# Optimization experiments

Measured on AMD Instinct MI355X. Metric: run time of the kernel, lower is better.

Reference implementation:

```python
import jax, jax.numpy as jnp
import numpy as np

D_MODEL = 768
N_HEADS = 12
D_HEAD = 64
WINDOW = 16
LOOK_BACK = 1
IGNORE = -1.0e6


def look_around(x, backward=LOOK_BACK, forward=0, pad_value=0):
    # x: (b, n_windows, w, ...) -> (b, n_windows, w*(backward+forward+1), ...)
    n = x.shape[1]
    pad = [(0, 0)] * x.ndim
    pad[1] = (backward, forward)
    px = jnp.pad(x, pad, constant_values=pad_value)
    return jnp.concatenate([px[:, i:i + n] for i in range(backward + forward + 1)], axis=2)


def setup_inputs() -> dict:
    key = jax.random.key(0)
    k1, k2, k3 = jax.random.split(key, 3)
    B, T = 2, 2048
    x = jax.random.normal(k1, (B, T, D_MODEL), dtype=jnp.float32)
    W_abcde = jax.random.normal(k2, (D_MODEL, 5 * N_HEADS * D_HEAD), dtype=jnp.float32) * (1.0 / np.sqrt(D_MODEL))
    b_abcde = jnp.zeros((5 * N_HEADS * D_HEAD,), dtype=jnp.float32)
    W_O = jax.random.normal(k3, (N_HEADS * D_HEAD, D_MODEL), dtype=jnp.float32) * (1.0 / np.sqrt(N_HEADS * D_HEAD))
    b_O = jnp.zeros((D_MODEL,), dtype=jnp.float32)
    return {"x": x, "W_abcde": W_abcde, "b_abcde": b_abcde, "W_O": W_O, "b_O": b_O}


def reference(x, W_abcde, b_abcde, W_O, b_O):
    B, T, _ = x.shape
    w = WINDOW
    nw = T // w
    Ww = w * (LOOK_BACK + 1)  # look-around window length

    abcde = x @ W_abcde + b_abcde                                    # (B,T,5*H*D)
    abcde = abcde.reshape(B, T, 5, N_HEADS, D_HEAD).transpose(2, 0, 3, 1, 4)  # (5,B,H,T,D)
    a, b, c, d, e = [t.reshape(B * N_HEADS, nw, w, D_HEAD) for t in abcde]
    a_l, b_l, d_l, e_l = (look_around(t) for t in (a, b, d, e))       # (BH,nw,Ww,D)

    # causal mask, same construction as get_causal_mask (pad_value=0)
    seq = jnp.arange(T).reshape(1, nw, w)
    bb = look_around(seq)                                            # (1,nw,Ww)
    # mask[n,m,l] = (seq_n < bb_l) | (bb_l <= bb_m)
    mask = (seq[..., :, None, None] < bb[..., None, None, :]) | (bb[..., None, None, :] <= bb[..., None, :, None])

    # third-order attention scores: (BH, nw, w, Ww, Ww)
    scores = jnp.einsum('bnwd,bnmd,bnld->bnwml', c, a_l, b_l)
    scores = jnp.where(mask, IGNORE, scores)
    scores = jnp.where(scores == 0, IGNORE, scores)
    probs = jax.nn.softmax((scores / D_HEAD).reshape(B * N_HEADS, nw, w, Ww * Ww), axis=-1)
    probs = probs.reshape(scores.shape)

    z = jnp.einsum('bnwml,bnmd->bnwd', probs, d_l) + jnp.einsum('bnwml,bnld->bnwd', probs, e_l)
    z = z.reshape(B, N_HEADS, nw, w, D_HEAD).transpose(0, 2, 3, 1, 4).reshape(B, T, N_HEADS * D_HEAD)
    return z @ W_O + b_O
```

## Files before the change

### kernel.cpp

```cpp
#include <hip/hip_runtime.h>

#define T_SEQ   2048
#define NHEADS  12
#define DHEAD   64
#define WIN     16
#define WW      32
#define NWIN    128
#define DMODEL  768
#define NABCDE  3840
#define IGNORE_V (-1.0e6f)
#define PAD_K   72
#define L2E64   0.022542110013890053f
#define IGN_SC  (-22542.110013890053f)

typedef float f32x4 __attribute__((ext_vector_type(4)));
typedef _Float16 f16x8 __attribute__((ext_vector_type(8)));

__device__ __forceinline__ short f2h(float f) {
    union { _Float16 h; short s; } u;
    u.h = (_Float16)f;
    return u.s;
}

__device__ __forceinline__ void gload_lds16(const short* g, short* l) {
    __builtin_amdgcn_global_load_lds(
        (const __attribute__((address_space(1))) void*)g,
        (__attribute__((address_space(3))) void*)l,
        16, 0, 0);
}

__global__ __launch_bounds__(256) void prep_kernel(
    const float* __restrict__ x, const float* __restrict__ W_abcde,
    const float* __restrict__ W_O,
    short* __restrict__ xh, short* __restrict__ Wt, short* __restrict__ WOt)
{
    __shared__ float tile[32][33];
    const int blk = blockIdx.x;
    const int tid = threadIdx.x;

    if (blk < 1536) {
        int i = (blk * 256 + tid) * 8;
        float4 a = *reinterpret_cast<const float4*>(&x[i]);
        float4 b = *reinterpret_cast<const float4*>(&x[i + 4]);
        union { short s[8]; uint4 u; } r;
        r.s[0] = f2h(a.x); r.s[1] = f2h(a.y); r.s[2] = f2h(a.z); r.s[3] = f2h(a.w);
        r.s[4] = f2h(b.x); r.s[5] = f2h(b.y); r.s[6] = f2h(b.z); r.s[7] = f2h(b.w);
        *reinterpret_cast<uint4*>(&xh[i]) = r.u;
        return;
    }
    const float* W; short* Wo; int N, bx, by;
    if (blk < 4416) {
        int t = blk - 1536;
        W = W_abcde; Wo = Wt; N = NABCDE;
        bx = (t % 120) * 32; by = (t / 120) * 32;
    } else {
        int t = blk - 4416;
        W = W_O; Wo = WOt; N = DMODEL;
        bx = (t % 24) * 32; by = (t / 24) * 32;
    }
    const int tx = tid & 31, ty = tid >> 5;
#pragma unroll
    for (int r = 0; r < 32; r += 8)
        tile[ty + r][tx] = W[(size_t)(by + ty + r) * N + bx + tx];
    __syncthreads();
#pragma unroll
    for (int r = 0; r < 32; r += 8)
        Wo[(size_t)(bx + ty + r) * DMODEL + by + tx] = f2h(tile[tx][ty + r]);
}

__global__ __launch_bounds__(512, 2) void gemm1_kernel(
    const short* __restrict__ A, const short* __restrict__ Bt,
    const float* __restrict__ bias, short* __restrict__ C,
    int M, int N, int K)
{
    __shared__ short LT[4][2][8192];

    const int tid  = threadIdx.x;
    const int wave = tid >> 6;
    const int lane = tid & 63;

    int bid = blockIdx.x;
    int t = (bid & 7) * 30 + (bid >> 3);
    const int bm = (t / 15) * 256;
    const int bn = (t % 15) * 256;

    const int wr = wave >> 2;
    const int wc = wave & 3;
    const int fm = lane & 15;
    const int ko = lane >> 4;
    const int kswz = ko ^ ((lane >> 2) & 3);
    const int w32 = wave * 32;

    const int srow = lane >> 2;
    const int scc  = ((lane & 3) ^ ((lane >> 4) & 3)) * 8;
    const short* gA[2]; const short* gB[2];
#pragma unroll
    for (int j = 0; j < 2; ++j) {
        gA[j] = A  + (size_t)(bm + w32 + j * 16 + srow) * K + scc;
        gB[j] = Bt + (size_t)(bn + w32 + j * 16 + srow) * K + scc;
    }

    f32x4 acc[8][4];
#pragma unroll
    for (int mi = 0; mi < 8; ++mi)
#pragma unroll
        for (int ni = 0; ni < 4; ++ni) acc[mi][ni] = (f32x4){0.f, 0.f, 0.f, 0.f};

#pragma unroll
    for (int kt = 0; kt < 3; ++kt) {
#pragma unroll
        for (int j = 0; j < 2; ++j) {
            gload_lds16(gA[j] + kt * 32, &LT[kt][0][(w32 + j * 16) * 32]);
            gload_lds16(gB[j] + kt * 32, &LT[kt][1][(w32 + j * 16) * 32]);
        }
    }

    const int NKT = K >> 5;
    const int nkm = NKT - 3;

#define G1_STEP(KB, VMC, DOSTAGE, KS)                                          \
    {                                                                          \
        asm volatile("s_waitcnt vmcnt(" #VMC ")" ::: "memory");                \
        __builtin_amdgcn_s_barrier();                                          \
        asm volatile("" ::: "memory");                                         \
        if (DOSTAGE) {                                                         \
            int sb_ = (KS) & 3;                                                \
            _Pragma("unroll")                                                  \
            for (int j = 0; j < 2; ++j) {                                      \
                gload_lds16(gA[j] + (KS) * 32, &LT[sb_][0][(w32 + j * 16) * 32]); \
                gload_lds16(gB[j] + (KS) * 32, &LT[sb_][1][(w32 + j * 16) * 32]); \
            }                                                                  \
        }                                                                      \
        const short* Ab_ = &LT[(KB)][0][0];                                    \
        const short* Bb_ = &LT[(KB)][1][0];                                    \
        f16x8 af_[8], bf_[4];                                                  \
        _Pragma("unroll")                                                      \
        for (int mi = 0; mi < 8; ++mi)                                         \
            af_[mi] = *reinterpret_cast<const f16x8*>(                         \
                &Ab_[(wr * 128 + mi * 16 + fm) * 32 + kswz * 8]);              \
        _Pragma("unroll")                                                      \
        for (int ni = 0; ni < 4; ++ni)                                         \
            bf_[ni] = *reinterpret_cast<const f16x8*>(                         \
                &Bb_[(wc * 64 + ni * 16 + fm) * 32 + kswz * 8]);               \
        __builtin_amdgcn_s_setprio(1);                                         \
        _Pragma("unroll")                                                      \
        for (int mi = 0; mi < 8; ++mi)                                         \
            _Pragma("unroll")                                                  \
            for (int ni = 0; ni < 4; ++ni)                                     \
                acc[mi][ni] = __builtin_amdgcn_mfma_f32_16x16x32_f16(          \
                    af_[mi], bf_[ni], acc[mi][ni], 0, 0, 0);                   \
        __builtin_amdgcn_s_setprio(0);                                         \
        asm volatile("" ::: "memory");                                         \
        __builtin_amdgcn_s_barrier();                                          \
    }

    for (int k = 0; k < nkm; ++k) {
        G1_STEP(k & 3, 8, true, k + 3);
    }
    G1_STEP(nkm & 3, 8, false, 0);
    G1_STEP((nkm + 1) & 3, 4, false, 0);
    G1_STEP((nkm + 2) & 3, 0, false, 0);
#undef G1_STEP

    float bv[4];
#pragma unroll
    for (int ni = 0; ni < 4; ++ni)
        bv[ni] = bias[bn + wc * 64 + ni * 16 + fm];

    short* cb = &LT[0][0][0];
#pragma unroll
    for (int half = 0; half < 2; ++half) {
        __syncthreads();
        if (wr == half) {
#pragma unroll
            for (int mi = 0; mi < 8; ++mi) {
#pragma unroll
                for (int r = 0; r < 4; ++r) {
                    int lrow = mi * 16 + ko * 4 + r;
#pragma unroll
                    for (int ni = 0; ni < 4; ++ni)
                        cb[lrow * 256 + wc * 64 + ni * 16 + fm] =
                            f2h(acc[mi][ni][r] + bv[ni]);
                }
            }
        }
        __syncthreads();
#pragma unroll
        for (int q = 0; q < 8; ++q) {
            int f = tid + q * 512;
            int row = f >> 5, c16 = (f & 31) * 8;
            *reinterpret_cast<uint4*>(
                &C[(size_t)(bm + half * 128 + row) * N + bn + c16]) =
                *reinterpret_cast<const uint4*>(&cb[row * 256 + c16]);
        }
    }
}

__global__ __launch_bounds__(256) void gemm_h16_64(
    const short* __restrict__ A, const short* __restrict__ Bt,
    const float* __restrict__ bias, float* __restrict__ C,
    int M, int N, int K)
{
    __shared__ short As[2][64 * 32];
    __shared__ short Bs[2][64 * 32];

    const int tid  = threadIdx.x;
    const int wave = tid >> 6;
    const int lane = tid & 63;
    const int bm = blockIdx.y * 64;
    const int bn = blockIdx.x * 64;

    const int st_row = lane >> 2;
    const int st_col = (lane & 3) * 8;
    const int fr_m = lane & 15;
    const int fr_k = (lane >> 4) * 8;
    const int wm = wave * 16;

    const short* gsrc[4];
    short* ldst[4];
#pragma unroll
    for (int j = 0; j < 4; ++j) {
        int c = wave * 4 + j;
        if (c < 8) {
            int kt = c >> 2, rg = c & 3;
            gsrc[j] = A + (size_t)(bm + rg * 16 + st_row) * K + kt * 32 + st_col;
            ldst[j] = &As[kt][(rg * 16) * 32];
        } else {
            int cb = c - 8;
            int kt = cb >> 2, rg = cb & 3;
            gsrc[j] = Bt + (size_t)(bn + rg * 16 + st_row) * K + kt * 32 + st_col;
            ldst[j] = &Bs[kt][(rg * 16) * 32];
        }
    }

    f32x4 acc[4];
#pragma unroll
    for (int ni = 0; ni < 4; ++ni) acc[ni] = (f32x4){0.f, 0.f, 0.f, 0.f};

    for (int k0 = 0; k0 < K; k0 += 64) {
#pragma unroll
        for (int j = 0; j < 4; ++j) gload_lds16(gsrc[j] + k0, ldst[j]);
        __syncthreads();

#pragma unroll
        for (int kt = 0; kt < 2; ++kt) {
            f16x8 af = *reinterpret_cast<const f16x8*>(
                &As[kt][(wm + fr_m) * 32 + fr_k]);
#pragma unroll
            for (int ni = 0; ni < 4; ++ni) {
                f16x8 bf = *reinterpret_cast<const f16x8*>(
                    &Bs[kt][(ni * 16 + fr_m) * 32 + fr_k]);
                acc[ni] = __builtin_amdgcn_mfma_f32_16x16x32_f16(
                    af, bf, acc[ni], 0, 0, 0);
            }
        }
        __syncthreads();
    }

    float bv[4];
#pragma unroll
    for (int ni = 0; ni < 4; ++ni)
        bv[ni] = bias[bn + ni * 16 + (lane & 15)];
    int rbase = bm + wm + (lane >> 4) * 4;
#pragma unroll
    for (int r = 0; r < 4; ++r) {
        size_t off = (size_t)(rbase + r) * N + bn + (lane & 15);
#pragma unroll
        for (int ni = 0; ni < 4; ++ni)
            C[off + ni * 16] = acc[ni][r] + bv[ni];
    }
}

__global__ __launch_bounds__(256) void attn_kernel(
    const short* __restrict__ abcde, short* __restrict__ z)
{
    const int blk = blockIdx.x;
    const int n  = blk & (NWIN - 1);
    const int bh = blk >> 7;
    const int b  = bh / NHEADS;
    const int h  = bh % NHEADS;

    __shared__ short sc[WIN * PAD_K];
    __shared__ short sa[WW * PAD_K];
    __shared__ short sb[WW * PAD_K];
    __shared__ short sd[WW * PAD_K];
    __shared__ short se[WW * PAD_K];
    __shared__ short epA[WIN * PAD_K];
    __shared__ float sinv[WIN];

    const int tid = threadIdx.x;
    const size_t rowbase = ((size_t)b * T_SEQ) * NABCDE;
    const int hd = h * DHEAD;

    if (tid < 128) {
        int row = tid >> 3, ch = (tid & 7) * 8;
        *reinterpret_cast<uint4*>(&sc[row * PAD_K + ch]) =
            *reinterpret_cast<const uint4*>(
                &abcde[rowbase + (size_t)(n * WIN + row) * NABCDE + 2 * DMODEL + hd + ch]);
    }
    {
        int row = tid >> 3, ch = (tid & 7) * 8;
        int t = n * WIN - WIN + row;
        uint4 va = {0u, 0u, 0u, 0u}, vb = va, vd = va, ve = va;
        if (t >= 0) {
            size_t base = rowbase + (size_t)t * NABCDE + hd + ch;
            va = *reinterpret_cast<const uint4*>(&abcde[base + 0 * DMODEL]);
            vb = *reinterpret_cast<const uint4*>(&abcde[base + 1 * DMODEL]);
            vd = *reinterpret_cast<const uint4*>(&abcde[base + 3 * DMODEL]);
            ve = *reinterpret_cast<const uint4*>(&abcde[base + 4 * DMODEL]);
        }
        *reinterpret_cast<uint4*>(&sa[row * PAD_K + ch]) = va;
        *reinterpret_cast<uint4*>(&sb[row * PAD_K + ch]) = vb;
        *reinterpret_cast<uint4*>(&sd[row * PAD_K + ch]) = vd;
        *reinterpret_cast<uint4*>(&se[row * PAD_K + ch]) = ve;
    }
    __syncthreads();

    const int wv = tid >> 6;
    const int lane = tid & 63;
    const int lc = lane & 15;
    const int ko = lane >> 4;

    f16x8 cfrag[2];
    f16x8 bfrag[2][2];
#pragma unroll
    for (int kt = 0; kt < 2; ++kt) {
        cfrag[kt] = *reinterpret_cast<const f16x8*>(
            &sc[(wv * 4 + (lc & 3)) * PAD_K + kt * 32 + ko * 8]) * (_Float16)L2E64;
        bfrag[0][kt] = *reinterpret_cast<const f16x8*>(&sb[lc * PAD_K + kt * 32 + ko * 8]);
        bfrag[1][kt] = *reinterpret_cast<const f16x8*>(&sb[(16 + lc) * PAD_K + kt * 32 + ko * 8]);
    }

    f32x4 acc[8][2];
#pragma unroll
    for (int mt = 0; mt < 8; ++mt) {
        acc[mt][0] = (f32x4){0.f, 0.f, 0.f, 0.f};
        acc[mt][1] = (f32x4){0.f, 0.f, 0.f, 0.f};
    }
    __builtin_amdgcn_s_setprio(1);
#pragma unroll
    for (int mt = 0; mt < 8; ++mt) {
#pragma unroll
        for (int kt = 0; kt < 2; ++kt) {
            f16x8 ar = *reinterpret_cast<const f16x8*>(
                &sa[(mt * 4 + (lc >> 2)) * PAD_K + kt * 32 + ko * 8]);
            f16x8 pa = cfrag[kt] * ar;
            acc[mt][0] = __builtin_amdgcn_mfma_f32_16x16x32_f16(pa, bfrag[0][kt], acc[mt][0], 0, 0, 0);
            acc[mt][1] = __builtin_amdgcn_mfma_f32_16x16x32_f16(pa, bfrag[1][kt], acc[mt][1], 0, 0, 0);
        }
    }
    __builtin_amdgcn_s_setprio(0);

    const int nbase = n * WIN;
    if (n != 0) {
#pragma unroll
        for (int lt = 0; lt < 2; ++lt) {
            const int l = lt * 16 + lc;
#pragma unroll
            for (int mt = 0; mt < 8; ++mt) {
                const bool mgt = l > (mt * 4 + ko);
#pragma unroll
                for (int reg = 0; reg < 4; ++reg) {
                    const bool keep = mgt && (wv * 4 + reg + WIN >= l);
                    float p = __builtin_amdgcn_exp2f(acc[mt][lt][reg]);
                    acc[mt][lt][reg] = keep ? p : 0.0f;
                }
            }
        }
    } else {
        int bbl_h[2]; bool keepL[2][4];
#pragma unroll
        for (int lt = 0; lt < 2; ++lt) {
            int l = lt * 16 + lc;
            bbl_h[lt] = (l < WIN) ? 0 : (l - WIN);
#pragma unroll
            for (int reg = 0; reg < 4; ++reg)
                keepL[lt][reg] = (wv * 4 + reg) >= bbl_h[lt];
        }
#pragma unroll
        for (int mt = 0; mt < 8; ++mt) {
            int m = mt * 4 + ko;
            int bbm = (m < WIN) ? 0 : (m - WIN);
#pragma unroll
            for (int lt = 0; lt < 2; ++lt) {
                bool mgt = bbl_h[lt] > bbm;
#pragma unroll
                for (int reg = 0; reg < 4; ++reg) {
                    float s = acc[mt][lt][reg];
                    if (!(keepL[lt][reg] && mgt) || s == 0.0f)
                        acc[mt][lt][reg] = IGN_SC;
                }
            }
        }
        float mx[4] = {-3.4e38f, -3.4e38f, -3.4e38f, -3.4e38f};
#pragma unroll
        for (int mt = 0; mt < 8; ++mt)
#pragma unroll
            for (int lt = 0; lt < 2; ++lt)
#pragma unroll
                for (int reg = 0; reg < 4; ++reg)
                    mx[reg] = fmaxf(mx[reg], acc[mt][lt][reg]);
#pragma unroll
        for (int reg = 0; reg < 4; ++reg) {
#pragma unroll
            for (int off = 1; off < 64; off <<= 1)
                mx[reg] = fmaxf(mx[reg], __shfl_xor(mx[reg], off, 64));
        }
#pragma unroll
        for (int mt = 0; mt < 8; ++mt)
#pragma unroll
            for (int lt = 0; lt < 2; ++lt)
#pragma unroll
                for (int reg = 0; reg < 4; ++reg)
                    acc[mt][lt][reg] = __builtin_amdgcn_exp2f(
                        acc[mt][lt][reg] - mx[reg]);
    }

    float plv[2][4];
#pragma unroll
    for (int lt = 0; lt < 2; ++lt) {
#pragma unroll
        for (int reg = 0; reg < 4; ++reg) {
            float p = acc[0][lt][reg];
#pragma unroll
            for (int mt = 1; mt < 8; ++mt) p += acc[mt][lt][reg];
            p += __shfl_xor(p, 16, 64);
            p += __shfl_xor(p, 32, 64);
            plv[lt][reg] = p;
        }
        float w  = (ko & 1) ? plv[lt][1] : plv[lt][0];
        float w2 = (ko & 1) ? plv[lt][3] : plv[lt][2];
        float ww = (ko & 2) ? w2 : w;
        epA[(wv * 4 + ko) * PAD_K + 32 + lt * 16 + lc] = f2h(ww);
    }

    {
        float s[4];
#pragma unroll
        for (int reg = 0; reg < 4; ++reg) {
            float t = plv[0][reg] + plv[1][reg];
            t += __shfl_xor(t, 1, 64);
            t += __shfl_xor(t, 2, 64);
            t += __shfl_xor(t, 4, 64);
            t += __shfl_xor(t, 8, 64);
            s[reg] = t;
        }
        if (lane == 0) {
#pragma unroll
            for (int reg = 0; reg < 4; ++reg) sinv[wv * 4 + reg] = 1.0f / s[reg];
        }
    }

    {
        float v8[8][4];
#pragma unroll
        for (int mt = 0; mt < 8; ++mt)
#pragma unroll
            for (int reg = 0; reg < 4; ++reg)
                v8[mt][reg] = acc[mt][0][reg] + acc[mt][1][reg];

        const bool s0 = lane & 1, s1 = lane & 2, s2 = lane & 4, s3 = lane & 8;
        float r1[4][4];
#pragma unroll
        for (int m2 = 0; m2 < 4; ++m2)
#pragma unroll
            for (int reg = 0; reg < 4; ++reg) {
                float u = v8[2 * m2][reg], w = v8[2 * m2 + 1][reg];
                float a = s0 ? w : u;
                float s = s0 ? u : w;
                r1[m2][reg] = a + __shfl_xor(s, 1, 64);
            }
        float r2[2][4];
#pragma unroll
        for (int m4 = 0; m4 < 2; ++m4)
#pragma unroll
            for (int reg = 0; reg < 4; ++reg) {
                float u = r1[2 * m4][reg], w = r1[2 * m4 + 1][reg];
                float a = s1 ? w : u;
                float s = s1 ? u : w;
                r2[m4][reg] = a + __shfl_xor(s, 2, 64);
            }
        float r3[4];
#pragma unroll
        for (int reg = 0; reg < 4; ++reg) {
            float u = r2[0][reg], w = r2[1][reg];
            float a = s2 ? w : u;
            float s = s2 ? u : w;
            r3[reg] = a + __shfl_xor(s, 4, 64);
        }
        float a0 = s3 ? r3[1] : r3[0];
        float q0 = s3 ? r3[0] : r3[1];
        float g0 = a0 + __shfl_xor(q0, 8, 64);
        float a1 = s3 ? r3[3] : r3[2];
        float q1 = s3 ? r3[2] : r3[3];
        float g1 = a1 + __shfl_xor(q1, 8, 64);

        int mcol = (lc & 7) * 4 + ko;
        int ib = wv * 4 + (lc >> 3);
        epA[ib * PAD_K + mcol]       = f2h(g0);
        epA[(ib + 2) * PAD_K + mcol] = f2h(g1);
    }

    const int dd = wv * 16 + lc;
    f16x8 bd, be;
    {
        unsigned dv[8], ev[8];
#pragma unroll
        for (int j = 0; j < 8; ++j) {
            dv[j] = *reinterpret_cast<const unsigned short*>(&sd[(ko * 8 + j) * PAD_K + dd]);
            ev[j] = *reinterpret_cast<const unsigned short*>(&se[(ko * 8 + j) * PAD_K + dd]);
        }
        union { unsigned u[4]; f16x8 v; } td, te;
#pragma unroll
        for (int j = 0; j < 4; ++j) {
            td.u[j] = __builtin_amdgcn_perm(dv[2 * j + 1], dv[2 * j], 0x05040100);
            te.u[j] = __builtin_amdgcn_perm(ev[2 * j + 1], ev[2 * j], 0x05040100);
        }
        bd = td.v; be = te.v;
    }
    __syncthreads();

    f16x8 apm = *reinterpret_cast<const f16x8*>(&epA[lc * PAD_K + ko * 8]);
    f16x8 apl = *reinterpret_cast<const f16x8*>(&epA[lc * PAD_K + 32 + ko * 8]);
    f32x4 zacc = (f32x4){0.f, 0.f, 0.f, 0.f};
    __builtin_amdgcn_s_setprio(1);
    zacc = __builtin_amdgcn_mfma_f32_16x16x32_f16(apm, bd, zacc, 0, 0, 0);
    zacc = __builtin_amdgcn_mfma_f32_16x16x32_f16(apl, be, zacc, 0, 0, 0);
    __builtin_amdgcn_s_setprio(0);

    short* zs = sd;
#pragma unroll
    for (int reg = 0; reg < 4; ++reg) {
        int i = ko * 4 + reg;
        zs[i * 64 + dd] = f2h(zacc[reg] * sinv[i]);
    }
    __syncthreads();
    {
        int row = tid >> 4;
        int ch  = (tid & 15) * 4;
        *reinterpret_cast<uint2*>(
            &z[((size_t)b * T_SEQ + nbase + row) * (NHEADS * DHEAD) + hd + ch]) =
            *reinterpret_cast<const uint2*>(&zs[row * 64 + ch]);
    }
}

extern "C" void kernel_launch(void* const* d_in, const int* in_sizes, int n_in,
                              void* d_out, int out_size, void* d_ws, size_t ws_size,
                              hipStream_t stream) {
    const float* x        = (const float*)d_in[0];
    const float* W_abcde  = (const float*)d_in[1];
    const float* b_abcde  = (const float*)d_in[2];
    const float* W_O      = (const float*)d_in[3];
    const float* b_O      = (const float*)d_in[4];
    float* out = (float*)d_out;

    char* ws = (char*)d_ws;
    short* abcde = (short*)ws;
    short* xh    = (short*)(ws + (size_t)31457280);
    short* Wt    = (short*)(ws + (size_t)31457280 + 6291456);
    short* WOt   = (short*)(ws + (size_t)31457280 + 6291456 + 5898240);
    short* zb    = xh;

    const int M = 2 * T_SEQ;

    prep_kernel<<<dim3(4992), dim3(256), 0, stream>>>(
        x, W_abcde, W_O, xh, Wt, WOt);

    gemm1_kernel<<<dim3(240), dim3(512), 0, stream>>>(
        xh, Wt, b_abcde, abcde, M, NABCDE, DMODEL);

    attn_kernel<<<dim3(2 * NHEADS * NWIN), dim3(256), 0, stream>>>(abcde, zb);

    gemm_h16_64<<<dim3(DMODEL / 64, M / 64), dim3(256), 0, stream>>>(
        zb, WOt, b_O, out, M, DMODEL, DMODEL);
}
```

Before: 147.9 us.

## Rewrite output projection GEMM with 128x64 tiles and 4-stage LDS pipeline

Replaces the 64x64 output-projection GEMM with a 128x64 tile kernel that keeps three k-slices in flight in a four-buffer LDS ring, using explicit vmcnt waits and barriers. It adds an XOR swizzle on LDS columns to avoid bank conflicts, a block-index remap for cache locality, and raises MFMA priority. The aim is to hide global-load latency and raise MFMA work per LDS read. In exchange it launches fewer blocks (384 vs 768), which can reduce occupancy, and it relies on hand-counted waitcnt values.

```diff
diff --git a/kernel.cpp b/kernel.cpp
--- a/kernel.cpp
+++ b/kernel.cpp
@@ -196,78 +196,116 @@
     }
 }
 
-__global__ __launch_bounds__(256) void gemm_h16_64(
+__global__ __launch_bounds__(256) void gemm2_kernel(
     const short* __restrict__ A, const short* __restrict__ Bt,
     const float* __restrict__ bias, float* __restrict__ C,
     int M, int N, int K)
 {
-    __shared__ short As[2][64 * 32];
-    __shared__ short Bs[2][64 * 32];
+    __shared__ short LT[4][6144];
 
     const int tid  = threadIdx.x;
     const int wave = tid >> 6;
     const int lane = tid & 63;
-    const int bm = blockIdx.y * 64;
-    const int bn = blockIdx.x * 64;
-
-    const int st_row = lane >> 2;
-    const int st_col = (lane & 3) * 8;
-    const int fr_m = lane & 15;
-    const int fr_k = (lane >> 4) * 8;
-    const int wm = wave * 16;
-
-    const short* gsrc[4];
-    short* ldst[4];
-#pragma unroll
-    for (int j = 0; j < 4; ++j) {
-        int c = wave * 4 + j;
+
+    int bid = blockIdx.x;
+    int t = (bid & 7) * 48 + (bid >> 3);
+    const int bm = (t / 12) * 128;
+    const int bn = (t % 12) * 64;
+
+    const int wr = wave >> 1;
+    const int wc = wave & 1;
+    const int fm = lane & 15;
+    const int ko = lane >> 4;
+    const int kswz = ko ^ ((lane >> 2) & 3);
+
+    const int srow = lane >> 2;
+    const int scc  = ((lane & 3) ^ ((lane >> 4) & 3)) * 8;
+
+    const short* gsrc[3];
+    int loff[3];
+#pragma unroll
+    for (int j = 0; j < 3; ++j) {
+        int c = wave * 3 + j;
         if (c < 8) {
-            int kt = c >> 2, rg = c & 3;
-            gsrc[j] = A + (size_t)(bm + rg * 16 + st_row) * K + kt * 32 + st_col;
-            ldst[j] = &As[kt][(rg * 16) * 32];
+            gsrc[j] = A + (size_t)(bm + c * 16 + srow) * K + scc;
+            loff[j] = (c * 16) * 32;
         } else {
             int cb = c - 8;
-            int kt = cb >> 2, rg = cb & 3;
-            gsrc[j] = Bt + (size_t)(bn + rg * 16 + st_row) * K + kt * 32 + st_col;
-            ldst[j] = &Bs[kt][(rg * 16) * 32];
-        }
-    }
-
-    f32x4 acc[4];
-#pragma unroll
-    for (int ni = 0; ni < 4; ++ni) acc[ni] = (f32x4){0.f, 0.f, 0.f, 0.f};
-
-    for (int k0 = 0; k0 < K; k0 += 64) {
-#pragma unroll
-        for (int j = 0; j < 4; ++j) gload_lds16(gsrc[j] + k0, ldst[j]);
-        __syncthreads();
-
-#pragma unroll
-        for (int kt = 0; kt < 2; ++kt) {
-            f16x8 af = *reinterpret_cast<const f16x8*>(
-                &As[kt][(wm + fr_m) * 32 + fr_k]);
-#pragma unroll
-            for (int ni = 0; ni < 4; ++ni) {
-                f16x8 bf = *reinterpret_cast<const f16x8*>(
-                    &Bs[kt][(ni * 16 + fr_m) * 32 + fr_k]);
-                acc[ni] = __builtin_amdgcn_mfma_f32_16x16x32_f16(
-                    af, bf, acc[ni], 0, 0, 0);
-            }
-        }
-        __syncthreads();
-    }
-
-    float bv[4];
-#pragma unroll
-    for (int ni = 0; ni < 4; ++ni)
-        bv[ni] = bias[bn + ni * 16 + (lane & 15)];
-    int rbase = bm + wm + (lane >> 4) * 4;
-#pragma unroll
-    for (int r = 0; r < 4; ++r) {
-        size_t off = (size_t)(rbase + r) * N + bn + (lane & 15);
-#pragma unroll
-        for (int ni = 0; ni < 4; ++ni)
-            C[off + ni * 16] = acc[ni][r] + bv[ni];
+            gsrc[j] = Bt + (size_t)(bn + cb * 16 + srow) * K + scc;
+            loff[j] = 4096 + (cb * 16) * 32;
+        }
+    }
+
+    f32x4 acc[4][2];
+#pragma unroll
+    for (int mi = 0; mi < 4; ++mi)
+#pragma unroll
+        for (int ni = 0; ni < 2; ++ni) acc[mi][ni] = (f32x4){0.f, 0.f, 0.f, 0.f};
+
+#pragma unroll
+    for (int kt = 0; kt < 3; ++kt)
+#pragma unroll
+        for (int j = 0; j < 3; ++j)
+            gload_lds16(gsrc[j] + kt * 32, &LT[kt][loff[j]]);
+
+    const int NKT = K >> 5;
+    const int nkm = NKT - 3;
+
+#define G2_STEP(KB, VMC, DOSTAGE, KS)                                          \
+    {                                                                          \
+        asm volatile("s_waitcnt vmcnt(" #VMC ")" ::: "memory");                \
+        __builtin_amdgcn_s_barrier();                                          \
+        asm volatile("" ::: "memory");                                         \
+        if (DOSTAGE) {                                                         \
+            int sb_ = (KS) & 3;                                                \
+            _Pragma("unroll")                                                  \
+            for (int j = 0; j < 3; ++j)                                        \
+                gload_lds16(gsrc[j] + (KS) * 32, &LT[sb_][loff[j]]);           \
+        }                                                                      \
+        const short* Lb_ = &LT[(KB)][0];                                       \
+        f16x8 af_[4], bf_[2];                                                  \
+        _Pragma("unroll")                                                      \
+        for (int mi = 0; mi < 4; ++mi)                                         \
+            af_[mi] = *reinterpret_cast<const f16x8*>(                         \
+                &Lb_[(wr * 64 + mi * 16 + fm) * 32 + kswz * 8]);               \
+        _Pragma("unroll")                                                      \
+        for (int ni = 0; ni < 2; ++ni)                                         \
+            bf_[ni] = *reinterpret_cast<const f16x8*>(                         \
+                &Lb_[4096 + (wc * 32 + ni * 16 + fm) * 32 + kswz * 8]);        \
+        __builtin_amdgcn_s_setprio(1);                                         \
+        _Pragma("unroll")                                                      \
+        for (int mi = 0; mi < 4; ++mi)                                         \
+            _Pragma("unroll")                                                  \
+            for (int ni = 0; ni < 2; ++ni)                                     \
+                acc[mi][ni] = __builtin_amdgcn_mfma_f32_16x16x32_f16(          \
+                    af_[mi], bf_[ni], acc[mi][ni], 0, 0, 0);                   \
+        __builtin_amdgcn_s_setprio(0);                                         \
+        asm volatile("" ::: "memory");                                         \
+        __builtin_amdgcn_s_barrier();                                          \
+    }
+
+    for (int k = 0; k < nkm; ++k) {
+        G2_STEP(k & 3, 6, true, k + 3);
+    }
+    G2_STEP(nkm & 3, 6, false, 0);
+    G2_STEP((nkm + 1) & 3, 3, false, 0);
+    G2_STEP((nkm + 2) & 3, 0, false, 0);
+#undef G2_STEP
+
+    float bv[2];
+#pragma unroll
+    for (int ni = 0; ni < 2; ++ni)
+        bv[ni] = bias[bn + wc * 32 + ni * 16 + fm];
+#pragma unroll
+    for (int mi = 0; mi < 4; ++mi) {
+#pragma unroll
+        for (int r = 0; r < 4; ++r) {
+            size_t off = (size_t)(bm + wr * 64 + mi * 16 + ko * 4 + r) * N
+                         + bn + wc * 32 + fm;
+#pragma unroll
+            for (int ni = 0; ni < 2; ++ni)
+                C[off + ni * 16] = acc[mi][ni][r] + bv[ni];
+        }
     }
 }
 
@@ -571,6 +609,6 @@
 
     attn_kernel<<<dim3(2 * NHEADS * NWIN), dim3(256), 0, stream>>>(abcde, zb);
 
-    gemm_h16_64<<<dim3(DMODEL / 64, M / 64), dim3(256), 0, stream>>>(
+    gemm2_kernel<<<dim3(384), dim3(256), 0, stream>>>(
         zb, WOt, b_O, out, M, DMODEL, DMODEL);
 }
```

Result: no change. 149.0 us (+0.8%).
